# Kernel optimization log

Measured on AMD Instinct MI355X. Metric: run time of the kernel, lower is better.

The kernel has to match this reference:

```python
import jax, jax.numpy as jnp
import numpy as np

# NTU spatial neighbor triples (1-indexed joint labels in the original repo; we
# subtract 1 to get valid 0-based indices into the J=25 joint axis).
_NTU = np.array([[17,1,13],[21,2,1],[4,3,21],[3,4,3],[21,5,6],[5,6,7],[6,7,8],
                 [7,8,7],[10,9,23],[11,10,9],[12,11,10],[25,12,11],[1,13,14],
                 [13,14,15],[14,15,16],[15,16,15],[18,17,1],[19,18,17],
                 [20,19,18],[19,20,19],[9,21,5],[23,22,23],[8,23,22],
                 [25,24,25],[24,25,12]], dtype=np.int32) - 1

B, C, J, T, CO = 64, 3, 25, 256, 64
SIG_C = 4 + 16 + 64  # (C+1) + (C+1)^2 + (C+1)^3 with time augmentation, depth 3
EPS = 1e-5


def _exp_levels(d):
    # truncated tensor exponential of a linear increment, depth 3
    d2 = jnp.einsum('ni,nj->nij', d, d)
    d3 = jnp.einsum('nij,nk->nijk', d2, d)
    return d, d2 * 0.5, d3 / 6.0


def _sig3(path):
    # path: (N, 3, c). Signature with basepoint=0 via Chen's relation, depth 3.
    incs = jnp.concatenate([path[:, :1, :], path[:, 1:, :] - path[:, :-1, :]], axis=1)
    S1, S2, S3 = _exp_levels(incs[:, 0])
    for t in range(1, incs.shape[1]):  # fixed small stream length (3)
        B1, B2, B3 = _exp_levels(incs[:, t])
        S3 = S3 + B3 + jnp.einsum('ni,njk->nijk', S1, B2) + jnp.einsum('nij,nk->nijk', S2, B1)
        S2 = S2 + B2 + jnp.einsum('ni,nj->nij', S1, B1)
        S1 = S1 + B1
    N = path.shape[0]
    return jnp.concatenate([S1, S2.reshape(N, -1), S3.reshape(N, -1)], axis=1)


def _signet(inp, W, b):
    # inp: (N, 3, C) -> augment with time in [0,1] (signatory.Augment include_time)
    N = inp.shape[0]
    time = jnp.broadcast_to(jnp.linspace(0.0, 1.0, 3, dtype=inp.dtype)[None, :, None], (N, 3, 1))
    aug = jnp.concatenate([time, inp], axis=-1)  # (N, 3, C+1)
    return _sig3(aug) @ W + b


def _bn(x, g, b):
    # training-mode BatchNorm2d (biased variance) over (B, H, W) per channel
    m = x.mean(axis=(0, 2, 3), keepdims=True)
    v = x.var(axis=(0, 2, 3), keepdims=True)
    return (x - m) * jax.lax.rsqrt(v + EPS) * g.reshape(1, -1, 1, 1) + b.reshape(1, -1, 1, 1)


def setup_inputs() -> dict:
    key = jax.random.key(0)
    ks = jax.random.split(key, 12)
    inp = {
        'x': jax.random.normal(ks[0], (B, C, J, T), jnp.float32),
        'conv_w': jax.random.normal(ks[1], (CO, C, 1, 3), jnp.float32) * 0.3,
        'conv_b': jax.random.normal(ks[2], (CO,), jnp.float32) * 0.05,
        'raw_gamma': jnp.ones((CO,), jnp.float32),
        'raw_beta': jnp.zeros((CO,), jnp.float32),
        'sp_W': jax.random.normal(ks[3], (SIG_C, CO), jnp.float32) * 0.1,
        'sp_b': jax.random.normal(ks[4], (CO,), jnp.float32) * 0.05,
        'tp_W': jax.random.normal(ks[5], (SIG_C, CO), jnp.float32) * 0.1,
        'tp_b': jax.random.normal(ks[6], (CO,), jnp.float32) * 0.05,
        'ps_w': jax.random.normal(ks[7], (CO, 2 * CO), jnp.float32) * 0.1,
        'ps_b': jax.random.normal(ks[8], (CO,), jnp.float32) * 0.05,
        'ps_gamma': jnp.ones((CO,), jnp.float32),
        'ps_beta': jnp.zeros((CO,), jnp.float32),
        'fu_w': jax.random.normal(ks[9], (CO, 2 * CO), jnp.float32) * 0.1,
        'fu_b': jax.random.normal(ks[10], (CO,), jnp.float32) * 0.05,
        'fu_gamma': jnp.ones((CO,), jnp.float32),
        'fu_beta': jnp.zeros((CO,), jnp.float32),
        'neighbors': jnp.asarray(_NTU, jnp.int32),
    }
    return inp


def reference(x, conv_w, conv_b, raw_gamma, raw_beta, sp_W, sp_b, tp_W, tp_b,
              ps_w, ps_b, ps_gamma, ps_beta, fu_w, fu_b, fu_gamma, fu_beta,
              neighbors):
    Bx, Cx, Jx, Tx = x.shape
    # --- raw branch: Conv2d (1,3) pad (0,1) -> ReLU -> BN ---
    x_conv = jax.lax.conv_general_dilated(
        x, conv_w, window_strides=(1, 1), padding=((0, 0), (1, 1)),
        dimension_numbers=('NCHW', 'OIHW', 'NCHW')) + conv_b.reshape(1, -1, 1, 1)
    x_conv = _bn(jax.nn.relu(x_conv), raw_gamma, raw_beta)

    # --- spatial paths: gather neighbor triples per joint ---
    # x[:, :, neighbors, :]: (B, C, J, 3, T) -> (J, B, T, 3, C)
    sp = jnp.transpose(x[:, :, neighbors, :], (2, 0, 4, 3, 1)).reshape(Jx * Bx * Tx, 3, Cx)
    spatial_sig = _signet(sp, sp_W, sp_b)  # (J*B*T, CO)
    spatial_sig = jnp.transpose(spatial_sig.reshape(Jx, Bx, Tx, CO), (1, 3, 0, 2))  # (B,CO,J,T)

    # --- temporal paths: sliding window of 3 with replicate padding ---
    x_ps = jnp.pad(x, ((0, 0), (0, 0), (0, 0), (1, 1)), mode='edge')  # (B,C,J,T+2)
    win = jnp.arange(Tx)[:, None] + jnp.arange(3)[None, :]  # (T, 3)
    xw = x_ps[:, :, :, win]  # (B, C, J, T, 3)
    tp = jnp.transpose(xw, (3, 0, 2, 4, 1)).reshape(Tx * Bx * Jx, 3, Cx)
    temporal_sig = _signet(tp, tp_W, tp_b)  # (T*B*J, CO)
    temporal_sig = jnp.transpose(temporal_sig.reshape(Tx, Bx, Jx, CO), (1, 3, 2, 0))  # (B,CO,J,T)

    # --- ps_fusion: 1x1 conv -> ReLU -> BN ---
    sig = jnp.concatenate([spatial_sig, temporal_sig], axis=1)  # (B, 2CO, J, T)
    sig = jnp.einsum('bihw,oi->bohw', sig, ps_w) + ps_b.reshape(1, -1, 1, 1)
    sig = _bn(jax.nn.relu(sig), ps_gamma, ps_beta)

    # --- final fusion with conv branch ---
    x_out = jnp.concatenate([x_conv, sig], axis=1)  # (B, 2CO, J, T)
    x_out = jnp.einsum('bihw,oi->bohw', x_out, fu_w) + fu_b.reshape(1, -1, 1, 1)
    x_out = _bn(jax.nn.relu(x_out), fu_gamma, fu_beta)
    return x_out
```

## Files before the change

### kernel.cpp

```cpp
#include <hip/hip_runtime.h>
#include <hip/hip_bf16.h>
#include <stdint.h>

#define B_   64
#define C_   3
#define J_   25
#define T_   256
#define CO_  64
#define N_   (B_*J_*T_)
#define SIGD 84
#define FSTR 177
#define ZSTR 133

__device__ __forceinline__ unsigned short f2b(float f) {
    unsigned int u = __float_as_uint(f);
    u += 0x7fffu + ((u >> 16) & 1u);
    return (unsigned short)(u >> 16);
}
__device__ __forceinline__ float b2f(unsigned int bits_lo16) {
    return __uint_as_float(bits_lo16 << 16);
}
__device__ __forceinline__ unsigned int pack2(float a, float b) {
    return (unsigned int)f2b(a) | ((unsigned int)f2b(b) << 16);
}

__device__ __forceinline__ void sig3(const float v0[4], const float v1[4],
                                     const float v2[4], float* __restrict__ S) {
    float* S1 = S;
    float* S2 = S + 4;
    float* S3 = S + 20;
    #pragma unroll
    for (int i = 0; i < 4; i++) S1[i] = v0[i];
    #pragma unroll
    for (int i = 0; i < 4; i++)
        #pragma unroll
        for (int j = 0; j < 4; j++) S2[i*4+j] = 0.5f * v0[i] * v0[j];
    #pragma unroll
    for (int i = 0; i < 4; i++)
        #pragma unroll
        for (int j = 0; j < 4; j++)
            #pragma unroll
            for (int k = 0; k < 4; k++)
                S3[i*16+j*4+k] = S2[i*4+j] * v0[k] * (1.f/3.f);

    #pragma unroll
    for (int s = 0; s < 2; s++) {
        const float* v = (s == 0) ? v1 : v2;
        float B2[16], v3[4];
        #pragma unroll
        for (int k = 0; k < 4; k++) v3[k] = v[k] * (1.f/3.f);
        #pragma unroll
        for (int i = 0; i < 4; i++)
            #pragma unroll
            for (int j = 0; j < 4; j++) B2[i*4+j] = 0.5f * v[i] * v[j];
        #pragma unroll
        for (int i = 0; i < 4; i++)
            #pragma unroll
            for (int j = 0; j < 4; j++)
                #pragma unroll
                for (int k = 0; k < 4; k++)
                    S3[i*16+j*4+k] += B2[i*4+j]*v3[k] + S1[i]*B2[j*4+k] + S2[i*4+j]*v[k];
        #pragma unroll
        for (int i = 0; i < 4; i++)
            #pragma unroll
            for (int j = 0; j < 4; j++) S2[i*4+j] += B2[i*4+j] + S1[i]*v[j];
        #pragma unroll
        for (int i = 0; i < 4; i++) S1[i] += v[i];
    }
}

__global__ void k_prep(const float* __restrict__ sp_W, const float* __restrict__ sp_b,
                       const float* __restrict__ tp_W, const float* __restrict__ tp_b,
                       const float* __restrict__ ps_w, const float* __restrict__ ps_b,
                       float* __restrict__ wsig_t, float* __restrict__ cb) {
    int k = blockIdx.x;
    int o = threadIdx.x;
    if (k < SIGD) {
        float v = 0.f;
        for (int i = 0; i < 64; i++) v += sp_W[k*64+i] * ps_w[o*128+i];
        wsig_t[k*64 + o] = v;
    } else if (k < 2*SIGD) {
        int m = k - SIGD;
        float v = 0.f;
        for (int i = 0; i < 64; i++) v += tp_W[m*64+i] * ps_w[o*128+64+i];
        wsig_t[k*64 + o] = v;
    } else {
        float a = ps_b[o];
        for (int i = 0; i < 64; i++)
            a += ps_w[o*128+i]*sp_b[i] + ps_w[o*128+64+i]*tp_b[i];
        cb[o] = a;
    }
}

__global__ __launch_bounds__(256) void k_sig(const float* __restrict__ x,
                                             const int* __restrict__ nbr,
                                             const float* __restrict__ wsig_t,
                                             const float* __restrict__ cb,
                                             const float* __restrict__ conv_w,
                                             const float* __restrict__ conv_b,
                                             unsigned short* __restrict__ zcat) {
    __shared__ float feats[64*FSTR];

    const int i       = threadIdx.x;
    const int quarter = blockIdx.x & 3;
    const int bj      = blockIdx.x >> 2;
    const int b       = bj / J_, j = bj % J_;
    const int loc_base = bj*T_ + quarter*64;

    if (i < 128) {
        const int lt   = i >> 1;
        const int path = i & 1;
        const int t    = quarter*64 + lt;
        float p0[4], p1[4], p2[4];
        p0[0] = 0.f; p1[0] = 0.5f; p2[0] = 1.0f;
        if (path == 0) {
            int n0 = nbr[j*3+0], n1 = nbr[j*3+1], n2 = nbr[j*3+2];
            #pragma unroll
            for (int c = 0; c < 3; c++) {
                const float* xc = x + ((size_t)(b*3+c)*J_)*T_ + t;
                p0[c+1] = xc[n0*T_];
                p1[c+1] = xc[n1*T_];
                p2[c+1] = xc[n2*T_];
            }
        } else {
            int tm = (t > 0)    ? t-1 : 0;
            int tp = (t < T_-1) ? t+1 : T_-1;
            #pragma unroll
            for (int c = 0; c < 3; c++) {
                const float* xr = x + ((size_t)(b*3+c)*J_ + j)*T_;
                p0[c+1] = xr[tm];
                p1[c+1] = xr[t];
                p2[c+1] = xr[tp];
            }
        }
        float v0[4], v1[4], v2[4];
        #pragma unroll
        for (int d = 0; d < 4; d++) { v0[d]=p0[d]; v1[d]=p1[d]-p0[d]; v2[d]=p2[d]-p1[d]; }
        float S[SIGD];
        sig3(v0, v1, v2, S);
        float* frow = feats + lt*FSTR + path*SIGD;
        #pragma unroll
        for (int m = 0; m < SIGD; m++) frow[m] = S[m];
    } else {
        const int ci  = i - 128;
        const int lt  = ci >> 1;
        const int chh = ci & 1;
        const int t   = quarter*64 + lt;
        const int loc = loc_base + lt;
        float xm[3], x0[3], xp[3];
        #pragma unroll
        for (int c = 0; c < 3; c++) {
            const float* xr = x + ((size_t)(b*3+c)*J_ + j)*T_;
            xm[c] = (t > 0)     ? xr[t-1] : 0.f;
            x0[c] = xr[t];
            xp[c] = (t < T_-1)  ? xr[t+1] : 0.f;
        }
        unsigned int packed[16];
        #pragma unroll
        for (int oo2 = 0; oo2 < 16; oo2++) {
            float r[2];
            #pragma unroll
            for (int e = 0; e < 2; e++) {
                int o = chh*32 + oo2*2 + e;
                float acc = conv_b[o];
                #pragma unroll
                for (int c = 0; c < 3; c++) {
                    const float* wr = conv_w + (o*3+c)*3;
                    acc += wr[0]*xm[c] + wr[1]*x0[c] + wr[2]*xp[c];
                }
                r[e] = fmaxf(acc, 0.f);
            }
            packed[oo2] = pack2(r[0], r[1]);
        }
        uint4* dst = (uint4*)(zcat + (size_t)loc*128 + chh*32);
        #pragma unroll
        for (int k = 0; k < 4; k++)
            dst[k] = make_uint4(packed[k*4+0], packed[k*4+1], packed[k*4+2], packed[k*4+3]);
    }
    __syncthreads();

    const int og = __builtin_amdgcn_readfirstlane(i >> 6);
    const int lt = i & 63;
    const int loc = loc_base + lt;
    const float* wt  = wsig_t + og*16;
    const float* cbp = cb + og*16;
    float acc[16];
    #pragma unroll
    for (int oo = 0; oo < 16; oo++) acc[oo] = cbp[oo];
    const float* frow = feats + lt*FSTR;
    #pragma unroll 4
    for (int k = 0; k < 2*SIGD; k++) {
        float f = frow[k];
        const float* w = wt + k*64;
        #pragma unroll
        for (int oo = 0; oo < 16; oo++) acc[oo] = fmaf(f, w[oo], acc[oo]);
    }
    unsigned int pk[8];
    #pragma unroll
    for (int p = 0; p < 8; p++)
        pk[p] = pack2(fmaxf(acc[2*p],0.f), fmaxf(acc[2*p+1],0.f));
    uint4* dst = (uint4*)(zcat + (size_t)loc*128 + 64 + og*16);
    dst[0] = make_uint4(pk[0], pk[1], pk[2], pk[3]);
    dst[1] = make_uint4(pk[4], pk[5], pk[6], pk[7]);
}

template<int NCH>
__global__ __launch_bounds__(256) void k_stats(const unsigned short* __restrict__ z,
                                               float* __restrict__ sum,
                                               float* __restrict__ ssq) {
    constexpr int G  = NCH/8;
    constexpr int LP = 256/G;
    const int i = threadIdx.x;
    const int g = i % G;
    const int lr = i / G;
    const int base = blockIdx.x * 1600;
    float s[8], qq[8];
    #pragma unroll
    for (int k = 0; k < 8; k++) { s[k] = 0.f; qq[k] = 0.f; }
    for (int l = lr; l < 1600; l += LP) {
        const uint4 v = *(const uint4*)(z + (size_t)(base + l)*NCH + g*8);
        unsigned int u[4] = { v.x, v.y, v.z, v.w };
        #pragma unroll
        for (int k = 0; k < 4; k++) {
            float f0 = b2f(u[k] & 0xffffu);
            float f1 = __uint_as_float(u[k] & 0xffff0000u);
            s[2*k]   += f0;  qq[2*k]   += f0*f0;
            s[2*k+1] += f1;  qq[2*k+1] += f1*f1;
        }
    }
    const int lane = i & 63, wv = i >> 6;
    for (int off = 32; off >= G; off >>= 1) {
        #pragma unroll
        for (int k = 0; k < 8; k++) {
            s[k]  += __shfl_down(s[k],  off);
            qq[k] += __shfl_down(qq[k], off);
        }
    }
    __shared__ float red[4][G][16];
    if (lane < G) {
        #pragma unroll
        for (int k = 0; k < 8; k++) { red[wv][lane][k] = s[k]; red[wv][lane][8+k] = qq[k]; }
    }
    __syncthreads();
    if (i < G*16) {
        int g2 = i >> 4, slot = i & 15;
        float v = red[0][g2][slot] + red[1][g2][slot] + red[2][g2][slot] + red[3][g2][slot];
        int ch = g2*8 + (slot & 7);
        atomicAdd((slot < 8 ? sum : ssq) + ch, v);
    }
}

__global__ void k_fin1(const float* __restrict__ sum_cp, const float* __restrict__ ssq_cp,
                       const float* __restrict__ raw_g, const float* __restrict__ raw_b,
                       const float* __restrict__ ps_g,  const float* __restrict__ ps_bt,
                       const float* __restrict__ fu_w,  const float* __restrict__ fu_b,
                       float* __restrict__ w12s_t, float* __restrict__ fb2) {
    __shared__ float a[128], d[128];
    int i = threadIdx.x;
    const float inv = 1.f / (float)N_;
    {
        float m = sum_cp[i]*inv, v = ssq_cp[i]*inv - m*m;
        float sc = rsqrtf(v + 1e-5f) * raw_g[i];
        a[i] = sc; d[i] = raw_b[i] - m*sc;
    }
    {
        float m = sum_cp[64+i]*inv, v = ssq_cp[64+i]*inv - m*m;
        float sc = rsqrtf(v + 1e-5f) * ps_g[i];
        a[64+i] = sc; d[64+i] = ps_bt[i] - m*sc;
    }
    __syncthreads();
    int o = i;
    float fb = fu_b[o];
    for (int k = 0; k < 128; k++) {
        float w = fu_w[o*128 + k];
        fb += w * d[k];
        w12s_t[k*64 + o] = w * a[k];
    }
    fb2[o] = fb;
}

__global__ __launch_bounds__(256) void k_fu(const unsigned short* __restrict__ zcat,
                                            const float* __restrict__ w12s_t,
                                            const float* __restrict__ fb2,
                                            unsigned short* __restrict__ z_fu) {
    __shared__ float zt[64*ZSTR];
    const int i = threadIdx.x;
    const int loc_base = blockIdx.x * 64;

    for (int c = i; c < 1024; c += 256) {
        int row = c >> 4, seg = c & 15;
        uint4 v = *(const uint4*)(zcat + (size_t)(loc_base + row)*128 + seg*8);
        float* drow = zt + row*ZSTR + seg*8;
        unsigned int u[4] = { v.x, v.y, v.z, v.w };
        #pragma unroll
        for (int e = 0; e < 4; e++) {
            drow[2*e]   = b2f(u[e] & 0xffffu);
            drow[2*e+1] = __uint_as_float(u[e] & 0xffff0000u);
        }
    }
    __syncthreads();

    const int og = __builtin_amdgcn_readfirstlane(i >> 6);
    const int lt = i & 63;
    const int loc = loc_base + lt;
    const float* wt  = w12s_t + og*16;
    const float* fbp = fb2 + og*16;
    float acc[16];
    #pragma unroll
    for (int oo = 0; oo < 16; oo++) acc[oo] = fbp[oo];
    const float* frow = zt + lt*ZSTR;
    #pragma unroll 4
    for (int k = 0; k < 128; k++) {
        float f = frow[k];
        const float* w = wt + k*64;
        #pragma unroll
        for (int oo = 0; oo < 16; oo++) acc[oo] = fmaf(f, w[oo], acc[oo]);
    }
    unsigned int pk[8];
    #pragma unroll
    for (int p = 0; p < 8; p++)
        pk[p] = pack2(fmaxf(acc[2*p],0.f), fmaxf(acc[2*p+1],0.f));
    uint4* dst = (uint4*)(z_fu + (size_t)loc*64 + og*16);
    dst[0] = make_uint4(pk[0], pk[1], pk[2], pk[3]);
    dst[1] = make_uint4(pk[4], pk[5], pk[6], pk[7]);
}

__global__ void k_fin2(const float* __restrict__ sum_f, const float* __restrict__ ssq_f,
                       const float* __restrict__ fu_g,
                       float* __restrict__ mf, float* __restrict__ rfg) {
    int o = threadIdx.x;
    const float inv = 1.f / (float)N_;
    float m = sum_f[o]*inv, v = ssq_f[o]*inv - m*m;
    mf[o] = m;
    rfg[o] = rsqrtf(v + 1e-5f) * fu_g[o];
}

__global__ __launch_bounds__(256) void k_out(const unsigned short* __restrict__ z_fu,
                                             const float* __restrict__ mf,
                                             const float* __restrict__ rfg,
                                             const float* __restrict__ fu_beta,
                                             float* __restrict__ out) {
    __shared__ __align__(16) unsigned short zt[256*66];
    const int i = threadIdx.x;
    const int bj = blockIdx.x;
    const int b = bj / J_, j = bj % J_;
    const int loc_base = bj * T_;

    for (int c = i; c < 2048; c += 256) {
        int row = c >> 3, k = c & 7;
        uint4 v = *(const uint4*)(z_fu + (size_t)(loc_base + row)*64 + k*8);
        unsigned int* dst = (unsigned int*)(zt + row*66 + k*8);
        dst[0] = v.x; dst[1] = v.y; dst[2] = v.z; dst[3] = v.w;
    }
    __syncthreads();

    const int t = i;
    const unsigned int* zrow = (const unsigned int*)zt + t*33;
    for (int o = 0; o < 64; o += 2) {
        unsigned int v = zrow[o >> 1];
        float f0 = b2f(v & 0xffffu);
        float f1 = __uint_as_float(v & 0xffff0000u);
        out[(((size_t)b*64 + o  )*J_ + j)*T_ + t] = (f0 - mf[o  ])*rfg[o  ] + fu_beta[o  ];
        out[(((size_t)b*64 + o+1)*J_ + j)*T_ + t] = (f1 - mf[o+1])*rfg[o+1] + fu_beta[o+1];
    }
}

extern "C" void kernel_launch(void* const* d_in, const int* in_sizes, int n_in,
                              void* d_out, int out_size, void* d_ws, size_t ws_size,
                              hipStream_t stream) {
    const float* x         = (const float*)d_in[0];
    const float* conv_w    = (const float*)d_in[1];
    const float* conv_b    = (const float*)d_in[2];
    const float* raw_gamma = (const float*)d_in[3];
    const float* raw_beta  = (const float*)d_in[4];
    const float* sp_W      = (const float*)d_in[5];
    const float* sp_b      = (const float*)d_in[6];
    const float* tp_W      = (const float*)d_in[7];
    const float* tp_b      = (const float*)d_in[8];
    const float* ps_w      = (const float*)d_in[9];
    const float* ps_b      = (const float*)d_in[10];
    const float* ps_gamma  = (const float*)d_in[11];
    const float* ps_beta   = (const float*)d_in[12];
    const float* fu_w      = (const float*)d_in[13];
    const float* fu_b      = (const float*)d_in[14];
    const float* fu_gamma  = (const float*)d_in[15];
    const float* fu_beta   = (const float*)d_in[16];
    const int*   neighbors = (const int*)d_in[17];

    char* ws = (char*)d_ws;
    unsigned short* zcat   = (unsigned short*)ws;
    unsigned short* z_fu   = (unsigned short*)(ws + 104857600);
    size_t off = 157286400;
    float* wsig_t = (float*)(ws + off); off += 168*64*4;
    float* w12s_t = (float*)(ws + off); off += 128*64*4;
    float* f32s   = (float*)(ws + off);
    float* cb     = f32s;
    float* fb2    = f32s + 64;
    float* mf     = f32s + 128;
    float* rfg    = f32s + 192;
    float* sum_cp = f32s + 256;
    float* ssq_cp = f32s + 384;
    float* sum_f  = f32s + 512;
    float* ssq_f  = f32s + 576;

    hipMemsetAsync(sum_cp, 0, 384*sizeof(float), stream);

    k_prep<<<169, 64, 0, stream>>>(sp_W, sp_b, tp_W, tp_b, ps_w, ps_b, wsig_t, cb);
    k_sig<<<6400, 256, 0, stream>>>(x, neighbors, wsig_t, cb, conv_w, conv_b, zcat);
    k_stats<128><<<256, 256, 0, stream>>>(zcat, sum_cp, ssq_cp);
    k_fin1<<<1, 64, 0, stream>>>(sum_cp, ssq_cp, raw_gamma, raw_beta,
                                 ps_gamma, ps_beta, fu_w, fu_b, w12s_t, fb2);
    k_fu<<<6400, 256, 0, stream>>>(zcat, w12s_t, fb2, z_fu);
    k_stats<64><<<256, 256, 0, stream>>>(z_fu, sum_f, ssq_f);
    k_fin2<<<1, 64, 0, stream>>>(sum_f, ssq_f, fu_gamma, mf, rfg);
    k_out<<<1600, 256, 0, stream>>>(z_fu, mf, rfg, fu_beta, (float*)d_out);
}
```

Measured before the change: 459.3 us.

## Use bf16 MFMA with split-weight precision for fusion 1x1 conv

Moves the k_fu 128->64 channel fusion GEMM from scalar FP32 FMAs to 16x16x32 bf16 MFMA instructions. Fused weights are split into high and low bf16 halves to keep near-FP32 accuracy, and each block now handles 128 locations with the bf16 activations staged in LDS directly. A runtime probe checks the MFMA output layout and falls back to a scalar path if the layout does not match. The k_sig epilogue is also changed to use packed float2 FMAs.

Measured after the change: 436.3 us. 1.05x faster.

```diff
diff --git a/kernel.cpp b/kernel.cpp
--- a/kernel.cpp
+++ b/kernel.cpp
@@ -10,7 +10,12 @@
 #define N_   (B_*J_*T_)
 #define SIGD 84
 #define FSTR 177
-#define ZSTR 133
+#define WST  136
+
+typedef short   s16x8  __attribute__((ext_vector_type(8)));
+typedef __bf16  bf16x8 __attribute__((ext_vector_type(8)));
+typedef float   f32x4  __attribute__((ext_vector_type(4)));
+typedef float   f32x2  __attribute__((ext_vector_type(2)));
 
 __device__ __forceinline__ unsigned short f2b(float f) {
     unsigned int u = __float_as_uint(f);
@@ -22,6 +27,10 @@
 }
 __device__ __forceinline__ unsigned int pack2(float a, float b) {
     return (unsigned int)f2b(a) | ((unsigned int)f2b(b) << 16);
+}
+__device__ __forceinline__ void split2(float f, unsigned short& h, unsigned short& l) {
+    h = f2b(f);
+    l = f2b(f - b2f((unsigned int)h));
 }
 
 __device__ __forceinline__ void sig3(const float v0[4], const float v1[4],
@@ -182,23 +191,26 @@
     const int og = __builtin_amdgcn_readfirstlane(i >> 6);
     const int lt = i & 63;
     const int loc = loc_base + lt;
-    const float* wt  = wsig_t + og*16;
-    const float* cbp = cb + og*16;
-    float acc[16];
-    #pragma unroll
-    for (int oo = 0; oo < 16; oo++) acc[oo] = cbp[oo];
+    const float* wt = wsig_t + og*16;
+    f32x2 acc2[8];
+    {
+        const f32x2* cbp = (const f32x2*)(cb + og*16);
+        #pragma unroll
+        for (int p = 0; p < 8; p++) acc2[p] = cbp[p];
+    }
     const float* frow = feats + lt*FSTR;
     #pragma unroll 4
     for (int k = 0; k < 2*SIGD; k++) {
         float f = frow[k];
-        const float* w = wt + k*64;
-        #pragma unroll
-        for (int oo = 0; oo < 16; oo++) acc[oo] = fmaf(f, w[oo], acc[oo]);
+        f32x2 f2 = { f, f };
+        const f32x2* w2 = (const f32x2*)(wt + k*64);
+        #pragma unroll
+        for (int p = 0; p < 8; p++) acc2[p] += f2 * w2[p];
     }
     unsigned int pk[8];
     #pragma unroll
     for (int p = 0; p < 8; p++)
-        pk[p] = pack2(fmaxf(acc[2*p],0.f), fmaxf(acc[2*p+1],0.f));
+        pk[p] = pack2(fmaxf(acc2[p][0],0.f), fmaxf(acc2[p][1],0.f));
     uint4* dst = (uint4*)(zcat + (size_t)loc*128 + 64 + og*16);
     dst[0] = make_uint4(pk[0], pk[1], pk[2], pk[3]);
     dst[1] = make_uint4(pk[4], pk[5], pk[6], pk[7]);
@@ -254,6 +266,7 @@
                        const float* __restrict__ raw_g, const float* __restrict__ raw_b,
                        const float* __restrict__ ps_g,  const float* __restrict__ ps_bt,
                        const float* __restrict__ fu_w,  const float* __restrict__ fu_b,
+                       unsigned short* __restrict__ w12h, unsigned short* __restrict__ w12l,
                        float* __restrict__ w12s_t, float* __restrict__ fb2) {
     __shared__ float a[128], d[128];
     int i = threadIdx.x;
@@ -274,55 +287,126 @@
     for (int k = 0; k < 128; k++) {
         float w = fu_w[o*128 + k];
         fb += w * d[k];
-        w12s_t[k*64 + o] = w * a[k];
-    }
+        float ws = w * a[k];
+        w12s_t[k*64 + o] = ws;
+        unsigned short h, l;
+        split2(ws, h, l);
+        w12h[o*WST + k] = h;
+        w12l[o*WST + k] = l;
+    }
+    for (int k = 128; k < WST; k++) { w12h[o*WST + k] = 0; w12l[o*WST + k] = 0; }
     fb2[o] = fb;
 }
 
 __global__ __launch_bounds__(256) void k_fu(const unsigned short* __restrict__ zcat,
+                                            const unsigned short* __restrict__ w12h,
+                                            const unsigned short* __restrict__ w12l,
                                             const float* __restrict__ w12s_t,
                                             const float* __restrict__ fb2,
                                             unsigned short* __restrict__ z_fu) {
-    __shared__ float zt[64*ZSTR];
+    __shared__ __align__(16) unsigned short zt[128*WST];
     const int i = threadIdx.x;
-    const int loc_base = blockIdx.x * 64;
-
-    for (int c = i; c < 1024; c += 256) {
-        int row = c >> 4, seg = c & 15;
-        uint4 v = *(const uint4*)(zcat + (size_t)(loc_base + row)*128 + seg*8);
-        float* drow = zt + row*ZSTR + seg*8;
-        unsigned int u[4] = { v.x, v.y, v.z, v.w };
-        #pragma unroll
-        for (int e = 0; e < 4; e++) {
-            drow[2*e]   = b2f(u[e] & 0xffffu);
-            drow[2*e+1] = __uint_as_float(u[e] & 0xffff0000u);
-        }
+    const int loc_base = blockIdx.x * 128;
+
+    for (int c = i; c < 2048; c += 256) {
+        int row = c >> 4, k = c & 15;
+        s16x8 v = *(const s16x8*)(zcat + (size_t)(loc_base + row)*128 + k*8);
+        *(s16x8*)(zt + row*WST + k*8) = v;
     }
     __syncthreads();
 
-    const int og = __builtin_amdgcn_readfirstlane(i >> 6);
-    const int lt = i & 63;
-    const int loc = loc_base + lt;
-    const float* wt  = w12s_t + og*16;
-    const float* fbp = fb2 + og*16;
-    float acc[16];
-    #pragma unroll
-    for (int oo = 0; oo < 16; oo++) acc[oo] = fbp[oo];
-    const float* frow = zt + lt*ZSTR;
-    #pragma unroll 4
-    for (int k = 0; k < 128; k++) {
-        float f = frow[k];
-        const float* w = wt + k*64;
-        #pragma unroll
-        for (int oo = 0; oo < 16; oo++) acc[oo] = fmaf(f, w[oo], acc[oo]);
-    }
-    unsigned int pk[8];
-    #pragma unroll
-    for (int p = 0; p < 8; p++)
-        pk[p] = pack2(fmaxf(acc[2*p],0.f), fmaxf(acc[2*p+1],0.f));
-    uint4* dst = (uint4*)(z_fu + (size_t)loc*64 + og*16);
-    dst[0] = make_uint4(pk[0], pk[1], pk[2], pk[3]);
-    dst[1] = make_uint4(pk[4], pk[5], pk[6], pk[7]);
+    const int lane = i & 63, wv = i >> 6;
+    const int mrow = lane & 15, q = lane >> 4;
+    const f32x4 zero = {0.f, 0.f, 0.f, 0.f};
+
+    bf16x8 ap, bp;
+    #pragma unroll
+    for (int jj = 0; jj < 8; jj++) { ap[jj] = (__bf16)(float)mrow; bp[jj] = (__bf16)1.0f; }
+    f32x4 pv = __builtin_amdgcn_mfma_f32_16x16x32_bf16(ap, bp, zero, 0, 0, 0);
+    bool cC = true, cT = true;
+    #pragma unroll
+    for (int r = 0; r < 4; r++) {
+        cC = cC && (pv[r] == 32.f*(float)(q*4 + r));
+        cT = cT && (pv[r] == 32.f*(float)mrow);
+    }
+    const bool okC = (__ballot(cC) == ~0ull);
+    const bool okT = (!okC) && (__ballot(cT) == ~0ull);
+
+    if (okC || okT) {
+        bf16x8 ah[4], al[4];
+        {
+            const unsigned short* arh = w12h + (size_t)(wv*16 + mrow)*WST + q*8;
+            const unsigned short* arl = w12l + (size_t)(wv*16 + mrow)*WST + q*8;
+            #pragma unroll
+            for (int s = 0; s < 4; s++) {
+                ah[s] = __builtin_bit_cast(bf16x8, *(const s16x8*)(arh + s*32));
+                al[s] = __builtin_bit_cast(bf16x8, *(const s16x8*)(arl + s*32));
+            }
+        }
+        f32x4 accs[8];
+        #pragma unroll
+        for (int lt8 = 0; lt8 < 8; lt8++) {
+            const unsigned short* brow = zt + (size_t)(lt8*16 + mrow)*WST + q*8;
+            f32x4 acc = zero;
+            #pragma unroll
+            for (int s = 0; s < 4; s++) {
+                bf16x8 bfrag = __builtin_bit_cast(bf16x8, *(const s16x8*)(brow + s*32));
+                acc = __builtin_amdgcn_mfma_f32_16x16x32_bf16(ah[s], bfrag, acc, 0, 0, 0);
+                acc = __builtin_amdgcn_mfma_f32_16x16x32_bf16(al[s], bfrag, acc, 0, 0, 0);
+            }
+            accs[lt8] = acc;
+        }
+        __syncthreads();
+
+        unsigned short* ot = zt;
+        if (okC) {
+            const float4 fbv = *(const float4*)(fb2 + wv*16 + q*4);
+            #pragma unroll
+            for (int lt8 = 0; lt8 < 8; lt8++) {
+                int row = lt8*16 + mrow;
+                int o   = wv*16 + q*4;
+                uint2 w;
+                w.x = pack2(fmaxf(accs[lt8][0]+fbv.x,0.f), fmaxf(accs[lt8][1]+fbv.y,0.f));
+                w.y = pack2(fmaxf(accs[lt8][2]+fbv.z,0.f), fmaxf(accs[lt8][3]+fbv.w,0.f));
+                *(uint2*)(ot + row*72 + o) = w;
+            }
+        } else {
+            const float fb1 = fb2[wv*16 + mrow];
+            #pragma unroll
+            for (int lt8 = 0; lt8 < 8; lt8++) {
+                #pragma unroll
+                for (int r = 0; r < 4; r++) {
+                    int row = lt8*16 + q*4 + r;
+                    ot[row*72 + wv*16 + mrow] = f2b(fmaxf(accs[lt8][r]+fb1, 0.f));
+                }
+            }
+        }
+        __syncthreads();
+        for (int c = i; c < 1024; c += 256) {
+            int row = c >> 3, k = c & 7;
+            s16x8 v = *(const s16x8*)(ot + row*72 + k*8);
+            *(s16x8*)(z_fu + (size_t)(loc_base + row)*64 + k*8) = v;
+        }
+    } else {
+        if (i < 128) {
+            const unsigned short* fr = zt + i*WST;
+            const int loc = loc_base + i;
+            for (int og8 = 0; og8 < 8; og8++) {
+                float acc[8];
+                #pragma unroll
+                for (int p = 0; p < 8; p++) acc[p] = fb2[og8*8 + p];
+                for (int k = 0; k < 128; k++) {
+                    float f = b2f(fr[k]);
+                    const float* w = w12s_t + k*64 + og8*8;
+                    #pragma unroll
+                    for (int p = 0; p < 8; p++) acc[p] = fmaf(f, w[p], acc[p]);
+                }
+                #pragma unroll
+                for (int p = 0; p < 8; p++)
+                    z_fu[(size_t)loc*64 + og8*8 + p] = f2b(fmaxf(acc[p], 0.f));
+            }
+        }
+    }
 }
 
 __global__ void k_fin2(const float* __restrict__ sum_f, const float* __restrict__ ssq_f,
@@ -391,8 +475,10 @@
     unsigned short* zcat   = (unsigned short*)ws;
     unsigned short* z_fu   = (unsigned short*)(ws + 104857600);
     size_t off = 157286400;
-    float* wsig_t = (float*)(ws + off); off += 168*64*4;
-    float* w12s_t = (float*)(ws + off); off += 128*64*4;
+    float* wsig_t = (float*)(ws + off);          off += 168*64*4;
+    float* w12s_t = (float*)(ws + off);          off += 128*64*4;
+    unsigned short* w12h = (unsigned short*)(ws + off); off += 64*WST*2;
+    unsigned short* w12l = (unsigned short*)(ws + off); off += 64*WST*2;
     float* f32s   = (float*)(ws + off);
     float* cb     = f32s;
     float* fb2    = f32s + 64;
@@ -409,8 +495,9 @@
     k_sig<<<6400, 256, 0, stream>>>(x, neighbors, wsig_t, cb, conv_w, conv_b, zcat);
     k_stats<128><<<256, 256, 0, stream>>>(zcat, sum_cp, ssq_cp);
     k_fin1<<<1, 64, 0, stream>>>(sum_cp, ssq_cp, raw_gamma, raw_beta,
-                                 ps_gamma, ps_beta, fu_w, fu_b, w12s_t, fb2);
-    k_fu<<<6400, 256, 0, stream>>>(zcat, w12s_t, fb2, z_fu);
+                                 ps_gamma, ps_beta, fu_w, fu_b,
+                                 w12h, w12l, w12s_t, fb2);
+    k_fu<<<3200, 256, 0, stream>>>(zcat, w12h, w12l, w12s_t, fb2, z_fu);
     k_stats<64><<<256, 256, 0, stream>>>(z_fu, sum_f, ssq_f);
     k_fin2<<<1, 64, 0, stream>>>(sum_f, ssq_f, fu_gamma, mf, rfg);
     k_out<<<1600, 256, 0, stream>>>(z_fu, mf, rfg, fu_beta, (float*)d_out);
```
